# Kernel tuning notes

Measured on AMD Instinct MI355X. Metric: run time of the kernel, lower is better.

Reference implementation:

```python
import jax, jax.numpy as jnp
import numpy as np

D_MODEL = 512; D_STATE = 64; D_CONV = 4; EXPAND = 2; HEADDIM = 64
D_INNER = EXPAND * D_MODEL          # 1024
NHEADS = D_INNER // HEADDIM         # 16
D_IN_PROJ = 2 * D_INNER + 2 * D_STATE + NHEADS  # z, xBC, dt
CONV_DIM = D_INNER + 2 * D_STATE
BETA = 0.5
BATCH = 8; SEQLEN = 1024
EPS_LN = 1e-12; EPS_RMS = 1e-5


def layernorm(x, w, b, eps=EPS_LN):
    mu = jnp.mean(x, axis=-1, keepdims=True)
    var = jnp.var(x, axis=-1, keepdims=True)
    return (x - mu) * jax.lax.rsqrt(var + eps) * w + b


def causal_dw_conv(x, w, b):
    # x: (b, l, c); w: (c, d_conv) depthwise; causal left-pad d_conv-1
    xt = jnp.transpose(x, (0, 2, 1))                 # (b, c, l)
    k = w[:, None, :]                                # (c, 1, d_conv)
    y = jax.lax.conv_general_dilated(
        xt, k, window_strides=(1,), padding=[(D_CONV - 1, 0)],
        feature_group_count=CONV_DIM,
        dimension_numbers=('NCH', 'OIH', 'NCH'))
    return jnp.transpose(y, (0, 2, 1)) + b


def ssd(x, dt, A, Bm, Cm, Dp):
    # x: (b,l,h,p)  dt: (b,l,h)  A: (h)  Bm,Cm: (b,l,n)  Dp: (h)
    dA = jnp.exp(dt * A)  # (b,l,h) decay per step

    def step(h, inp):
        dA_t, dt_t, B_t, C_t, x_t = inp
        # h: (b, heads, p, n)
        h = h * dA_t[:, :, None, None] + jnp.einsum('bh,bn,bhp->bhpn', dt_t, B_t, x_t)
        y = jnp.einsum('bhpn,bn->bhp', h, C_t)
        return h, y

    init = jnp.zeros((x.shape[0], NHEADS, HEADDIM, D_STATE), x.dtype)
    xs = (jnp.moveaxis(dA, 1, 0), jnp.moveaxis(dt, 1, 0),
          jnp.moveaxis(Bm, 1, 0), jnp.moveaxis(Cm, 1, 0), jnp.moveaxis(x, 1, 0))
    _, ys = jax.lax.scan(step, init, xs)
    y = jnp.moveaxis(ys, 0, 1)           # (b,l,h,p)
    return y + x * Dp[None, None, :, None]


def mamba2(u, in_proj_w, conv_w, conv_b, dt_bias, A_log, Dp, norm_w, out_proj_w):
    zxbcdt = u @ in_proj_w.T                                   # (b,l,D_IN_PROJ)
    z, xBC, dt = jnp.split(zxbcdt, [D_INNER, D_INNER + CONV_DIM], axis=-1)
    dt = jax.nn.softplus(dt + dt_bias)                          # (b,l,h)
    xBC = jax.nn.silu(causal_dw_conv(xBC, conv_w, conv_b))
    x, Bm, Cm = jnp.split(xBC, [D_INNER, D_INNER + D_STATE], axis=-1)
    x = x.reshape(x.shape[0], x.shape[1], NHEADS, HEADDIM)
    A = -jnp.exp(A_log)
    y = ssd(x, dt, A, Bm, Cm, Dp)
    y = y.reshape(y.shape[0], y.shape[1], D_INNER)
    g = y * jax.nn.silu(z)                                      # gated RMSNorm
    g = g * jax.lax.rsqrt(jnp.mean(g * g, axis=-1, keepdims=True) + EPS_RMS) * norm_w
    return g @ out_proj_w.T


def ffn(x, w1, b1, w2, b2, lnw, lnb):
    h = jax.nn.gelu(x @ w1.T + b1, approximate=False)
    h = h @ w2.T + b2
    return layernorm(h + x, lnw, lnb)


def setup_inputs() -> dict:
    key = jax.random.key(0)
    ks = jax.random.split(key, 12)
    item_emb = jax.random.normal(ks[0], (BATCH, SEQLEN, D_MODEL), jnp.float32)
    item_idx = jnp.zeros((BATCH, SEQLEN), jnp.int32)          # single sequence per row
    flip_index = jnp.arange(SEQLEN - 1, -1, -1, dtype=jnp.int64)
    s = 0.02
    in_proj_w = jax.random.normal(ks[1], (D_IN_PROJ, D_MODEL), jnp.float32) * s
    conv_w = jax.random.uniform(ks[2], (CONV_DIM, D_CONV), jnp.float32, -0.5, 0.5)
    conv_b = jnp.zeros((CONV_DIM,), jnp.float32)
    # dt_bias = inverse softplus of dt ~ U[1e-3, 0.1] in log space (mamba init)
    dt = jnp.exp(jax.random.uniform(ks[3], (NHEADS,), jnp.float32,
                                    np.log(1e-3), np.log(0.1)))
    dt_bias = dt + jnp.log(-jnp.expm1(-dt))
    A_log = jnp.log(jax.random.uniform(ks[4], (NHEADS,), jnp.float32, 1.0, 16.0))
    Dp = jnp.ones((NHEADS,), jnp.float32)
    norm_w = jnp.ones((D_INNER,), jnp.float32)
    out_proj_w = jax.random.normal(ks[5], (D_MODEL, D_INNER), jnp.float32) * s
    ln_w = jnp.ones((D_MODEL,), jnp.float32); ln_b = jnp.zeros((D_MODEL,), jnp.float32)
    ffn_w1 = jax.random.normal(ks[6], (4 * D_MODEL, D_MODEL), jnp.float32) * s
    ffn_b1 = jnp.zeros((4 * D_MODEL,), jnp.float32)
    ffn_w2 = jax.random.normal(ks[7], (D_MODEL, 4 * D_MODEL), jnp.float32) * s
    ffn_b2 = jnp.zeros((D_MODEL,), jnp.float32)
    ffn_ln_w = jnp.ones((D_MODEL,), jnp.float32); ffn_ln_b = jnp.zeros((D_MODEL,), jnp.float32)
    return dict(item_emb=item_emb, item_idx=item_idx, flip_index=flip_index,
                in_proj_w=in_proj_w, conv_w=conv_w, conv_b=conv_b, dt_bias=dt_bias,
                A_log=A_log, Dp=Dp, norm_w=norm_w, out_proj_w=out_proj_w,
                ln_w=ln_w, ln_b=ln_b, ffn_w1=ffn_w1, ffn_b1=ffn_b1,
                ffn_w2=ffn_w2, ffn_b2=ffn_b2, ffn_ln_w=ffn_ln_w, ffn_ln_b=ffn_ln_b)


def reference(item_emb, item_idx, flip_index, in_proj_w, conv_w, conv_b, dt_bias,
              A_log, Dp, norm_w, out_proj_w, ln_w, ln_b,
              ffn_w1, ffn_b1, ffn_w2, ffn_b2, ffn_ln_w, ffn_ln_b):
    # item_idx (seq_idx) is all-zeros -> no state resets; dropout is eval-mode identity.
    params = (in_proj_w, conv_w, conv_b, dt_bias, A_log, Dp, norm_w, out_proj_w)
    fwd = mamba2(item_emb, *params)
    bwd = mamba2(item_emb[:, flip_index, :], *params)   # shared weights, as in source
    h = fwd + bwd * BETA + item_emb
    h = layernorm(h, ln_w, ln_b)
    return ffn(h, ffn_w1, ffn_b1, ffn_w2, ffn_b2, ffn_ln_w, ffn_ln_b)
```

## Files before the change

### kernel.cpp

```cpp
#include <hip/hip_runtime.h>
#include <math.h>

#define SEQ     1024
#define NBATCH  8
#define NTOK    8192
#define DMODEL  512
#define DINNER  1024
#define NHEADS  16
#define DPROJ   2192
#define DPROJP  2304
#define CONVDIM 1152
#define DFFN    2048

typedef short bf16x8 __attribute__((ext_vector_type(8)));
typedef float f32x4  __attribute__((ext_vector_type(4)));

__device__ inline unsigned short f2bf(float f) {
  union { float f; unsigned int u; } v; v.f = f;
  unsigned int u = v.u;
  return (unsigned short)((u + 0x7FFFu + ((u >> 16) & 1u)) >> 16);
}
__device__ inline float bf2f(unsigned short s) {
  union { unsigned int u; float f; } v; v.u = ((unsigned int)s) << 16;
  return v.f;
}

#define GLDS16(g, l)                                                         \
  __builtin_amdgcn_global_load_lds(                                          \
      (const __attribute__((address_space(1))) unsigned int*)(g),            \
      (__attribute__((address_space(3))) unsigned int*)(l), 16, 0, 0)

__global__ __launch_bounds__(256) void cvt_bf16(const float* __restrict__ s,
                                                unsigned short* __restrict__ d, int n) {
  int i = blockIdx.x * 256 + threadIdx.x;
  if (i < n) d[i] = f2bf(s[i]);
}

__global__ __launch_bounds__(256) void cvt_bf16_pad(const float* __restrict__ s,
                                                    unsigned short* __restrict__ d,
                                                    int realrows, int cols, int padrows) {
  int i = blockIdx.x * 256 + threadIdx.x;
  if (i < padrows * cols) {
    int r = i / cols;
    d[i] = (r < realrows) ? f2bf(s[i]) : (unsigned short)0;
  }
}

template <int MODE>
__global__ __launch_bounds__(256)
void gemm_bt(const unsigned short* __restrict__ A, const unsigned short* __restrict__ B,
             void* __restrict__ Cout, const float* __restrict__ bias,
             float* __restrict__ aux, int Ksub, int lda, int Nreal, size_t zstrideC) {
  __shared__ unsigned short sA[2][128 * 32];
  __shared__ unsigned short sB[2][128 * 32];
  const int tid = threadIdx.x;
  const int bx = blockIdx.x, by = blockIdx.y, bz = blockIdx.z;
  const int lane = tid & 63;
  const int wave = tid >> 6;
  const int wm = wave >> 1, wn = wave & 1;
  const int arow = tid >> 2;
  const int acol = (tid & 3) << 3;

  const unsigned short* pA = A + (size_t)(by * 128 + arow) * lda + bz * Ksub + acol;
  const unsigned short* pB = B + (size_t)(bx * 128 + arow) * lda + bz * Ksub + acol;
  const size_t stride64 = (size_t)64 * lda;
  char* sAw[2] = { (char*)&sA[0][0] + wave * 1024, (char*)&sA[1][0] + wave * 1024 };
  char* sBw[2] = { (char*)&sB[0][0] + wave * 1024, (char*)&sB[1][0] + wave * 1024 };

  f32x4 acc[4][4];
#pragma unroll
  for (int i = 0; i < 4; i++)
#pragma unroll
    for (int j = 0; j < 4; j++) { f32x4 z = {0.f, 0.f, 0.f, 0.f}; acc[i][j] = z; }

  GLDS16(pA, sAw[0]);
  GLDS16(pA + stride64, sAw[0] + 4096);
  GLDS16(pB, sBw[0]);
  GLDS16(pB + stride64, sBw[0] + 4096);
  pA += 32; pB += 32;
  __syncthreads();

  const int lrow = lane & 15;
  const int lkq = (lane >> 4) << 3;
  int cur = 0;
  for (int k0 = 0; k0 < Ksub; k0 += 32) {
    if (k0 + 32 < Ksub) {
      const int nxt = cur ^ 1;
      GLDS16(pA, sAw[nxt]);
      GLDS16(pA + stride64, sAw[nxt] + 4096);
      GLDS16(pB, sBw[nxt]);
      GLDS16(pB + stride64, sBw[nxt] + 4096);
      pA += 32; pB += 32;
    }
    bf16x8 af[4], bfr[4];
#pragma unroll
    for (int mi = 0; mi < 4; mi++)
      af[mi] = *(const bf16x8*)&sA[cur][(wm * 64 + mi * 16 + lrow) * 32 + lkq];
#pragma unroll
    for (int ni = 0; ni < 4; ni++)
      bfr[ni] = *(const bf16x8*)&sB[cur][(wn * 64 + ni * 16 + lrow) * 32 + lkq];
#pragma unroll
    for (int mi = 0; mi < 4; mi++)
#pragma unroll
      for (int ni = 0; ni < 4; ni++)
        acc[mi][ni] = __builtin_amdgcn_mfma_f32_16x16x32_bf16(af[mi], bfr[ni], acc[mi][ni], 0, 0, 0);
    __syncthreads();
    cur ^= 1;
  }

  const int row0 = by * 128 + wm * 64;
  const int col0 = bx * 128 + wn * 64;
  float* outf = (float*)Cout;
  unsigned short* outp16 = (unsigned short*)Cout + (size_t)bz * zstrideC;
#pragma unroll
  for (int mi = 0; mi < 4; mi++) {
#pragma unroll
    for (int ni = 0; ni < 4; ni++) {
      const int col = col0 + ni * 16 + lrow;
      if (col < Nreal) {
        const float bval = (MODE == 0 || MODE == 1) && bias ? bias[col] : 0.f;
#pragma unroll
        for (int r = 0; r < 4; r++) {
          const int row = row0 + mi * 16 + ((lane >> 4) << 2) + r;
          float v = acc[mi][ni][r] + bval;
          if (MODE == 1) {
            float g = 0.5f * v * (1.f + erff(v * 0.7071067811865476f));
            ((unsigned short*)Cout)[(size_t)row * Nreal + col] = f2bf(g);
          } else if (MODE == 2) {
            ((unsigned short*)Cout)[(size_t)row * Nreal + col] = f2bf(v);
            if (col >= 2176) aux[(size_t)row * 16 + (col - 2176)] = v;
          } else if (MODE == 3) {
            outp16[(size_t)row * Nreal + col] = f2bf(v);
          } else {
            outf[(size_t)row * Nreal + col] = v;
          }
        }
      }
    }
  }
}

__global__ __launch_bounds__(256)
void dt_softplus(const float* __restrict__ zdt, const float* __restrict__ dt_bias,
                 float* __restrict__ dtf, float* __restrict__ dtb) {
  int i = blockIdx.x * 256 + threadIdx.x;
  int dir = i >> 17;
  int rem = i & 131071;
  int row = rem >> 10;
  int t = rem & 1023;
  int b = row >> 4, h = row & 15;
  int srow = (b << 10) + (dir ? (1023 - t) : t);
  float v = zdt[(size_t)srow * 16 + h] + dt_bias[h];
  float dt = (v > 20.f) ? v : log1pf(expf(v));
  (dir ? dtb : dtf)[(row << 10) + t] = dt;
}

__global__ __launch_bounds__(256)
void conv_silu_bf(const unsigned short* __restrict__ zxb, const float* __restrict__ cw,
                  const float* __restrict__ cb,
                  unsigned short* __restrict__ xcf, unsigned short* __restrict__ xcb) {
  const int tid = threadIdx.x;
  const int c = blockIdx.x * 128 + (tid & 127);
  const int b = blockIdx.y;
  const int seg = blockIdx.z * 2 + (tid >> 7);
  const int t0 = seg << 5;
  const float w0 = cw[c * 4 + 0], w1 = cw[c * 4 + 1], w2 = cw[c * 4 + 2], w3 = cw[c * 4 + 3];
  const float bias = cb[c];
  const unsigned short* src = zxb + (size_t)(b << 10) * DPROJ + DINNER + c;
  unsigned short* dstf = xcf + (size_t)(b << 10) * CONVDIM + c;
  unsigned short* dstb = xcb + (size_t)(b << 10) * CONVDIM + c;
  float r0 = 0.f, r1 = 0.f, r2 = 0.f;
  if (t0 >= 3) {
    r0 = bf2f(src[(size_t)(t0 - 3) * DPROJ]);
    r1 = bf2f(src[(size_t)(t0 - 2) * DPROJ]);
    r2 = bf2f(src[(size_t)(t0 - 1) * DPROJ]);
  }
  for (int s = t0; s < t0 + 32; s++) {
    float x = bf2f(src[(size_t)s * DPROJ]);
    float vf = bias + w0 * r0 + w1 * r1 + w2 * r2 + w3 * x;
    dstf[(size_t)s * CONVDIM] = f2bf(vf / (1.f + expf(-vf)));
    int tp = 1026 - s;
    if (tp <= 1023) {
      float vb = bias + w0 * x + w1 * r2 + w2 * r1 + w3 * r0;
      dstb[(size_t)tp * CONVDIM] = f2bf(vb / (1.f + expf(-vb)));
    }
    r0 = r1; r1 = r2; r2 = x;
  }
  if (seg == 31) {
    float v2 = bias + w1 * r2 + w2 * r1 + w3 * r0;
    float v1 = bias + w2 * r2 + w3 * r1;
    float v0 = bias + w3 * r2;
    dstb[(size_t)2 * CONVDIM] = f2bf(v2 / (1.f + expf(-v2)));
    dstb[(size_t)1 * CONVDIM] = f2bf(v1 / (1.f + expf(-v1)));
    dstb[0] = f2bf(v0 / (1.f + expf(-v0)));
  }
}

__global__ __launch_bounds__(256)
void ssd_chunk(const unsigned short* __restrict__ xcf, const unsigned short* __restrict__ xcb,
               const float* __restrict__ dtf, const float* __restrict__ dtb,
               const float* __restrict__ A_log, const float* __restrict__ Dp,
               unsigned short* __restrict__ yf, unsigned short* __restrict__ yb) {
  const int blk = blockIdx.x;
  const int dir = blk >> 7;
  const int b = (blk >> 4) & 7;
  const int h = blk & 15;
  const unsigned short* xc = dir ? xcb : xcf;
  const float* dts = (dir ? dtb : dtf) + ((size_t)((b << 4) + h) << 10);
  unsigned short* yo = dir ? yb : yf;
  const float A = -expf(A_log[h]);
  const float Dh = Dp[h];
  const int tid = threadIdx.x;
  const int lane = tid & 63;
  const int w = tid >> 6;
  const int lrow = lane & 15;
  const int quad = lane >> 4;
  const int lk8 = quad << 3;
  const int bS = b << 10;
  const int pr = tid & 31;
  const int sg = tid >> 5;

  __shared__ unsigned short Cb[64 * 72];
  __shared__ unsigned short Bb[64 * 72];
  __shared__ unsigned short Xt[64 * 72];
  __shared__ unsigned short Bt[64 * 72];
  __shared__ unsigned short Mb[64 * 72];
  __shared__ unsigned short Hb[64 * 72];
  __shared__ float sdt_all[1024];

  {
    float4 dv = *(const float4*)(dts + tid * 4);
    *(float4*)&sdt_all[tid * 4] = dv;
  }

  f32x4 hacc[4];
#pragma unroll
  for (int j = 0; j < 4; j++) { f32x4 z = {0.f, 0.f, 0.f, 0.f}; hacc[j] = z; }

  for (int c = 0; c < 16; c++) {
    const int t0 = c << 6;
    __syncthreads();

    float dtl = sdt_all[t0 + lane];
    float v = dtl;
#pragma unroll
    for (int off = 1; off < 64; off <<= 1) {
      float o = __shfl_up(v, off);
      if (lane >= off) v += o;
    }
    const float Lv = A * v;
    const float ev = expf(Lv);
    const float LL = __shfl(Lv, 63);
    const float wv = dtl * expf(LL - Lv);
    const float dtot = expf(LL);

#pragma unroll
    for (int j = 0; j < 4; j++)
#pragma unroll
      for (int r = 0; r < 4; r++)
        Hb[(w * 16 + quad * 4 + r) * 72 + j * 16 + lrow] = f2bf(hacc[j][r]);

#pragma unroll
    for (int pass = 0; pass < 2; pass++) {
      int u = pass * 256 + tid;
      int sl = u >> 3, c8 = u & 7;
      const unsigned short* rowp = xc + (size_t)(bS + t0 + sl) * CONVDIM;
      uint4 vb = *(const uint4*)(rowp + 1024 + c8 * 8);
      uint4 vc = *(const uint4*)(rowp + 1088 + c8 * 8);
      *(uint4*)&Bb[sl * 72 + c8 * 8] = vb;
      *(uint4*)&Cb[sl * 72 + c8 * 8] = vc;
    }

    {
      unsigned int xv[8], bv[8];
      const unsigned short* base = xc + (size_t)(bS + t0 + sg * 8) * CONVDIM;
#pragma unroll
      for (int k = 0; k < 8; k++) {
        const unsigned short* rp = base + (size_t)k * CONVDIM;
        xv[k] = *(const unsigned int*)(rp + h * 64 + pr * 2);
        bv[k] = *(const unsigned int*)(rp + 1024 + pr * 2);
      }
      unsigned short x0[8], x1[8], b0[8], b1[8];
#pragma unroll
      for (int k = 0; k < 8; k++) {
        float ws = __shfl(wv, sg * 8 + k);
        x0[k] = (unsigned short)(xv[k] & 0xffff);
        x1[k] = (unsigned short)(xv[k] >> 16);
        b0[k] = f2bf(bf2f((unsigned short)(bv[k] & 0xffff)) * ws);
        b1[k] = f2bf(bf2f((unsigned short)(bv[k] >> 16)) * ws);
      }
      *(uint4*)&Xt[(pr * 2 + 0) * 72 + sg * 8] = *(const uint4*)x0;
      *(uint4*)&Xt[(pr * 2 + 1) * 72 + sg * 8] = *(const uint4*)x1;
      *(uint4*)&Bt[(pr * 2 + 0) * 72 + sg * 8] = *(const uint4*)b0;
      *(uint4*)&Bt[(pr * 2 + 1) * 72 + sg * 8] = *(const uint4*)b1;
    }
    __syncthreads();

    f32x4 m1[4];
#pragma unroll
    for (int j = 0; j < 4; j++) { f32x4 z = {0.f, 0.f, 0.f, 0.f}; m1[j] = z; }
#pragma unroll
    for (int kq = 0; kq < 2; kq++) {
      bf16x8 af = *(const bf16x8*)&Cb[(w * 16 + lrow) * 72 + kq * 32 + lk8];
#pragma unroll
      for (int j = 0; j < 4; j++) {
        bf16x8 bf = *(const bf16x8*)&Bb[(j * 16 + lrow) * 72 + kq * 32 + lk8];
        m1[j] = __builtin_amdgcn_mfma_f32_16x16x32_bf16(af, bf, m1[j], 0, 0, 0);
      }
    }
#pragma unroll
    for (int r = 0; r < 4; r++) {
      int i = w * 16 + quad * 4 + r;
      float Li = __shfl(Lv, i);
#pragma unroll
      for (int j = 0; j < 4; j++) {
        int s = j * 16 + lrow;
        float Ls = __shfl(Lv, s);
        float ds = __shfl(dtl, s);
        float val = (s <= i) ? m1[j][r] * expf(Li - Ls) * ds : 0.f;
        Mb[i * 72 + s] = f2bf(val);
      }
    }
    __syncthreads();

    f32x4 Y[4], T[4], S[4];
#pragma unroll
    for (int j = 0; j < 4; j++) {
      f32x4 z = {0.f, 0.f, 0.f, 0.f};
      Y[j] = z; T[j] = z; S[j] = z;
    }
#pragma unroll
    for (int kq = 0; kq < 2; kq++) {
      bf16x8 am = *(const bf16x8*)&Mb[(w * 16 + lrow) * 72 + kq * 32 + lk8];
      bf16x8 ac = *(const bf16x8*)&Cb[(w * 16 + lrow) * 72 + kq * 32 + lk8];
      bf16x8 ax = *(const bf16x8*)&Xt[(w * 16 + lrow) * 72 + kq * 32 + lk8];
#pragma unroll
      for (int j = 0; j < 4; j++) {
        bf16x8 bx = *(const bf16x8*)&Xt[(j * 16 + lrow) * 72 + kq * 32 + lk8];
        bf16x8 bh = *(const bf16x8*)&Hb[(j * 16 + lrow) * 72 + kq * 32 + lk8];
        bf16x8 bw = *(const bf16x8*)&Bt[(j * 16 + lrow) * 72 + kq * 32 + lk8];
        Y[j] = __builtin_amdgcn_mfma_f32_16x16x32_bf16(am, bx, Y[j], 0, 0, 0);
        T[j] = __builtin_amdgcn_mfma_f32_16x16x32_bf16(ac, bh, T[j], 0, 0, 0);
        S[j] = __builtin_amdgcn_mfma_f32_16x16x32_bf16(ax, bw, S[j], 0, 0, 0);
      }
    }

#pragma unroll
    for (int r = 0; r < 4; r++) {
      int i = w * 16 + quad * 4 + r;
      float ei = __shfl(ev, i);
#pragma unroll
      for (int j = 0; j < 4; j++) {
        int p = j * 16 + lrow;
        float yv = Y[j][r] + ei * T[j][r] + Dh * bf2f(Xt[p * 72 + i]);
        yo[(size_t)(bS + t0 + i) * DINNER + h * 64 + p] = f2bf(yv);
      }
    }
#pragma unroll
    for (int j = 0; j < 4; j++)
#pragma unroll
      for (int r = 0; r < 4; r++)
        hacc[j][r] = dtot * hacc[j][r] + S[j][r];
  }
}

__device__ inline float2 block_sum2_256(float a, float b) {
#pragma unroll
  for (int o = 32; o >= 1; o >>= 1) { a += __shfl_xor(a, o); b += __shfl_xor(b, o); }
  __shared__ float ra[4], rb[4];
  const int lane = threadIdx.x & 63, w = threadIdx.x >> 6;
  if (lane == 0) { ra[w] = a; rb[w] = b; }
  __syncthreads();
  float2 out;
  out.x = ra[0] + ra[1] + ra[2] + ra[3];
  out.y = rb[0] + rb[1] + rb[2] + rb[3];
  return out;
}

__global__ __launch_bounds__(256)
void gate_rms_comb(const unsigned short* __restrict__ yf, const unsigned short* __restrict__ yb,
                   const unsigned short* __restrict__ zxb, const float* __restrict__ nw,
                   unsigned short* __restrict__ comb) {
  const int bt = blockIdx.x;
  const int b = bt >> 10, t = bt & 1023;
  const int zrowb = (b << 10) + (1023 - t);
  const int tid = threadIdx.x;
  ushort4 yf4 = *(const ushort4*)(yf + (size_t)bt * DINNER + tid * 4);
  ushort4 yb4 = *(const ushort4*)(yb + (size_t)bt * DINNER + tid * 4);
  ushort4 zf4 = *(const ushort4*)(zxb + (size_t)bt * DPROJ + tid * 4);
  ushort4 zb4 = *(const ushort4*)(zxb + (size_t)zrowb * DPROJ + tid * 4);
  float gf[4], gb[4];
  {
    float z0 = bf2f(zf4.x), z1 = bf2f(zf4.y), z2 = bf2f(zf4.z), z3 = bf2f(zf4.w);
    gf[0] = bf2f(yf4.x) * (z0 / (1.f + expf(-z0)));
    gf[1] = bf2f(yf4.y) * (z1 / (1.f + expf(-z1)));
    gf[2] = bf2f(yf4.z) * (z2 / (1.f + expf(-z2)));
    gf[3] = bf2f(yf4.w) * (z3 / (1.f + expf(-z3)));
  }
  {
    float z0 = bf2f(zb4.x), z1 = bf2f(zb4.y), z2 = bf2f(zb4.z), z3 = bf2f(zb4.w);
    gb[0] = bf2f(yb4.x) * (z0 / (1.f + expf(-z0)));
    gb[1] = bf2f(yb4.y) * (z1 / (1.f + expf(-z1)));
    gb[2] = bf2f(yb4.z) * (z2 / (1.f + expf(-z2)));
    gb[3] = bf2f(yb4.w) * (z3 / (1.f + expf(-z3)));
  }
  float2 sr = block_sum2_256(gf[0]*gf[0] + gf[1]*gf[1] + gf[2]*gf[2] + gf[3]*gf[3],
                             gb[0]*gb[0] + gb[1]*gb[1] + gb[2]*gb[2] + gb[3]*gb[3]);
  float sf = rsqrtf(sr.x * (1.f / 1024.f) + 1e-5f);
  float sb = 0.5f * rsqrtf(sr.y * (1.f / 1024.f) + 1e-5f);
  float4 wv = *(const float4*)(nw + tid * 4);
  unsigned short* o = comb + (size_t)bt * DINNER + tid * 4;
  o[0] = f2bf((gf[0] * sf + gb[0] * sb) * wv.x);
  o[1] = f2bf((gf[1] * sf + gb[1] * sb) * wv.y);
  o[2] = f2bf((gf[2] * sf + gb[2] * sb) * wv.z);
  o[3] = f2bf((gf[3] * sf + gb[3] * sb) * wv.w);
}

__global__ __launch_bounds__(256)
void combine_ln(const unsigned short* __restrict__ mo, const float* __restrict__ u,
                const float* __restrict__ w, const float* __restrict__ bias,
                float* __restrict__ hln, unsigned short* __restrict__ hbf) {
  const int bt = blockIdx.x;
  const int tid = threadIdx.x;
  const float2 uu = *(const float2*)(u + (size_t)bt * DMODEL + tid * 2);
  float vx = uu.x, vy = uu.y;
#pragma unroll
  for (int z = 0; z < 4; z++) {
    ushort2 p = *(const ushort2*)(mo + (size_t)z * NTOK * DMODEL + (size_t)bt * DMODEL + tid * 2);
    vx += bf2f(p.x);
    vy += bf2f(p.y);
  }
  float2 sr = block_sum2_256(vx + vy, vx * vx + vy * vy);
  float mean = sr.x * (1.f / 512.f);
  float var = sr.y * (1.f / 512.f) - mean * mean;
  float inv = rsqrtf(var + 1e-12f);
  float2 wv = *(const float2*)(w + tid * 2);
  float2 bv = *(const float2*)(bias + tid * 2);
  float ox = (vx - mean) * inv * wv.x + bv.x;
  float oy = (vy - mean) * inv * wv.y + bv.y;
  *(float2*)(hln + (size_t)bt * DMODEL + tid * 2) = make_float2(ox, oy);
  hbf[(size_t)bt * DMODEL + tid * 2] = f2bf(ox);
  hbf[(size_t)bt * DMODEL + tid * 2 + 1] = f2bf(oy);
}

__global__ __launch_bounds__(256)
void final_ln(const unsigned short* __restrict__ f2, const float* __restrict__ b2,
              const float* __restrict__ hln,
              const float* __restrict__ w, const float* __restrict__ bias,
              float* __restrict__ outp) {
  const int bt = blockIdx.x;
  const int tid = threadIdx.x;
  const float2 bb = *(const float2*)(b2 + tid * 2);
  const float2 h = *(const float2*)(hln + (size_t)bt * DMODEL + tid * 2);
  float vx = bb.x + h.x;
  float vy = bb.y + h.y;
#pragma unroll
  for (int z = 0; z < 4; z++) {
    ushort2 p = *(const ushort2*)(f2 + (size_t)z * NTOK * DMODEL + (size_t)bt * DMODEL + tid * 2);
    vx += bf2f(p.x);
    vy += bf2f(p.y);
  }
  float2 sr = block_sum2_256(vx + vy, vx * vx + vy * vy);
  float mean = sr.x * (1.f / 512.f);
  float var = sr.y * (1.f / 512.f) - mean * mean;
  float inv = rsqrtf(var + 1e-12f);
  float2 wv = *(const float2*)(w + tid * 2);
  float2 bv = *(const float2*)(bias + tid * 2);
  *(float2*)(outp + (size_t)bt * DMODEL + tid * 2) =
      make_float2((vx - mean) * inv * wv.x + bv.x, (vy - mean) * inv * wv.y + bv.y);
}

extern "C" void kernel_launch(void* const* d_in, const int* in_sizes, int n_in,
                              void* d_out, int out_size, void* d_ws, size_t ws_size,
                              hipStream_t stream) {
  const float* item_emb   = (const float*)d_in[0];
  const float* in_proj_w  = (const float*)d_in[3];
  const float* conv_w     = (const float*)d_in[4];
  const float* conv_b     = (const float*)d_in[5];
  const float* dt_bias    = (const float*)d_in[6];
  const float* A_log      = (const float*)d_in[7];
  const float* Dp         = (const float*)d_in[8];
  const float* norm_w     = (const float*)d_in[9];
  const float* out_proj_w = (const float*)d_in[10];
  const float* ln_w       = (const float*)d_in[11];
  const float* ln_b       = (const float*)d_in[12];
  const float* w1         = (const float*)d_in[13];
  const float* b1         = (const float*)d_in[14];
  const float* w2         = (const float*)d_in[15];
  const float* b2         = (const float*)d_in[16];
  const float* fln_w      = (const float*)d_in[17];
  const float* fln_b      = (const float*)d_in[18];
  float* outp = (float*)d_out;
  char* ws = (char*)d_ws;

  const size_t o_ubf  = 0;
  const size_t o_win  = 8388608;
  const size_t o_wout = 10747904;
  const size_t o_w1   = 11796480;
  const size_t o_w2   = 13893632;
  const size_t o_dtf  = 15990784;
  const size_t o_dtb  = 16515072;
  const size_t o_zdt  = 17039360;
  const size_t o_zxb  = 17563648;
  const size_t o_xcf  = 53477376;
  const size_t o_xcb  = 72351744;
  const size_t o_yf   = 91226112;
  const size_t o_yb   = 108003328;
  const size_t o_comb = o_xcf;
  const size_t o_mo   = o_zxb;
  const size_t o_hln  = o_yb;
  const size_t o_hbf  = o_ubf;
  const size_t o_h1   = o_xcb;
  const size_t o_f2   = o_zxb;

  unsigned short* u_bf  = (unsigned short*)(ws + o_ubf);
  unsigned short* winb  = (unsigned short*)(ws + o_win);
  unsigned short* woutb = (unsigned short*)(ws + o_wout);
  unsigned short* w1b   = (unsigned short*)(ws + o_w1);
  unsigned short* w2b   = (unsigned short*)(ws + o_w2);
  float* dtf = (float*)(ws + o_dtf);
  float* dtb = (float*)(ws + o_dtb);
  float* zdt = (float*)(ws + o_zdt);
  unsigned short* zxb = (unsigned short*)(ws + o_zxb);
  unsigned short* xcf = (unsigned short*)(ws + o_xcf);
  unsigned short* xcb = (unsigned short*)(ws + o_xcb);
  unsigned short* yf  = (unsigned short*)(ws + o_yf);
  unsigned short* yb  = (unsigned short*)(ws + o_yb);
  unsigned short* comb = (unsigned short*)(ws + o_comb);
  unsigned short* mo  = (unsigned short*)(ws + o_mo);
  float* hln = (float*)(ws + o_hln);
  unsigned short* hbf = (unsigned short*)(ws + o_hbf);
  unsigned short* h1b = (unsigned short*)(ws + o_h1);
  unsigned short* f2  = (unsigned short*)(ws + o_f2);

  {
    int n = NTOK * DMODEL;
    cvt_bf16<<<(n + 255) / 256, 256, 0, stream>>>(item_emb, u_bf, n);
    cvt_bf16_pad<<<(DPROJP * DMODEL + 255) / 256, 256, 0, stream>>>(in_proj_w, winb, DPROJ, DMODEL, DPROJP);
    n = DMODEL * DINNER;
    cvt_bf16<<<(n + 255) / 256, 256, 0, stream>>>(out_proj_w, woutb, n);
    n = DFFN * DMODEL;
    cvt_bf16<<<(n + 255) / 256, 256, 0, stream>>>(w1, w1b, n);
    n = DMODEL * DFFN;
    cvt_bf16<<<(n + 255) / 256, 256, 0, stream>>>(w2, w2b, n);
  }

  gemm_bt<2><<<dim3(DPROJP / 128, NTOK / 128), 256, 0, stream>>>(
      u_bf, winb, zxb, nullptr, zdt, DMODEL, DMODEL, DPROJ, 0);

  dt_softplus<<<1024, 256, 0, stream>>>(zdt, dt_bias, dtf, dtb);
  conv_silu_bf<<<dim3(9, NBATCH, 16), 256, 0, stream>>>(zxb, conv_w, conv_b, xcf, xcb);

  ssd_chunk<<<256, 256, 0, stream>>>(xcf, xcb, dtf, dtb, A_log, Dp, yf, yb);

  gate_rms_comb<<<NTOK, 256, 0, stream>>>(yf, yb, zxb, norm_w, comb);

  gemm_bt<3><<<dim3(DMODEL / 128, NTOK / 128, 4), 256, 0, stream>>>(
      comb, woutb, mo, nullptr, nullptr, DINNER / 4, DINNER, DMODEL,
      (size_t)NTOK * DMODEL);

  combine_ln<<<NTOK, 256, 0, stream>>>(mo, item_emb, ln_w, ln_b, hln, hbf);

  gemm_bt<1><<<dim3(DFFN / 128, NTOK / 128), 256, 0, stream>>>(
      hbf, w1b, h1b, b1, nullptr, DMODEL, DMODEL, DFFN, 0);

  gemm_bt<3><<<dim3(DMODEL / 128, NTOK / 128, 4), 256, 0, stream>>>(
      h1b, w2b, f2, nullptr, nullptr, DFFN / 4, DFFN, DMODEL,
      (size_t)NTOK * DMODEL);

  final_ln<<<NTOK, 256, 0, stream>>>(f2, b2, hln, fln_w, fln_b, outp);

  (void)in_sizes; (void)n_in; (void)out_size; (void)ws_size;
}
```

Measured before the change: 382.7 us.

## Double-buffer SSD chunk staging and split work across eight waves

The SSD chunk kernel now runs with 512 threads. Each wave computes half the output columns of a 16-row strip. Per-chunk cumsum, decay and weight values for all 16 chunks are computed up front into shared memory, replacing the per-chunk shuffles. The next chunk's B/C/X data is prefetched into registers and written into a second shared-memory buffer while the current chunk computes, which removes one barrier per chunk and hides global load latency. The cost is more shared memory per block and more per-thread register pressure.

Result: faster. 365.6 us (-4.5%).

```diff
diff --git a/kernel.cpp b/kernel.cpp
--- a/kernel.cpp
+++ b/kernel.cpp
@@ -196,7 +196,7 @@
   }
 }
 
-__global__ __launch_bounds__(256)
+__global__ __launch_bounds__(512)
 void ssd_chunk(const unsigned short* __restrict__ xcf, const unsigned short* __restrict__ xcb,
                const float* __restrict__ dtf, const float* __restrict__ dtb,
                const float* __restrict__ A_log, const float* __restrict__ Dp,
@@ -213,35 +213,56 @@
   const int tid = threadIdx.x;
   const int lane = tid & 63;
   const int w = tid >> 6;
+  const int wm = w >> 1;
+  const int wn = w & 1;
   const int lrow = lane & 15;
   const int quad = lane >> 4;
   const int lk8 = quad << 3;
   const int bS = b << 10;
+
+  __shared__ unsigned short Cb[2][64 * 72];
+  __shared__ unsigned short Bb[2][64 * 72];
+  __shared__ unsigned short Xt[2][64 * 72];
+  __shared__ unsigned short Bt[2][64 * 72];
+  __shared__ unsigned short Hb[2][64 * 72];
+  __shared__ unsigned short Mb[64 * 72];
+  __shared__ float sdt_all[1024];
+  __shared__ float Lv_all[16][64];
+  __shared__ float ev_all[16][64];
+  __shared__ float wv_all[16][64];
+  __shared__ float dtot_all[16];
+
+  const unsigned short* bcrow = xc + (size_t)(bS + (tid >> 3)) * CONVDIM + (tid & 7) * 8;
   const int pr = tid & 31;
   const int sg = tid >> 5;
-
-  __shared__ unsigned short Cb[64 * 72];
-  __shared__ unsigned short Bb[64 * 72];
-  __shared__ unsigned short Xt[64 * 72];
-  __shared__ unsigned short Bt[64 * 72];
-  __shared__ unsigned short Mb[64 * 72];
-  __shared__ unsigned short Hb[64 * 72];
-  __shared__ float sdt_all[1024];
-
+  const unsigned short* trow = xc + (size_t)(bS + sg * 4) * CONVDIM;
+
+  uint4 vb, vc;
+  unsigned int xv[4], bv[4];
+
+  vb = *(const uint4*)(bcrow + 1024);
+  vc = *(const uint4*)(bcrow + 1088);
   {
-    float4 dv = *(const float4*)(dts + tid * 4);
-    *(float4*)&sdt_all[tid * 4] = dv;
-  }
-
-  f32x4 hacc[4];
-#pragma unroll
-  for (int j = 0; j < 4; j++) { f32x4 z = {0.f, 0.f, 0.f, 0.f}; hacc[j] = z; }
-
-  for (int c = 0; c < 16; c++) {
-    const int t0 = c << 6;
-    __syncthreads();
-
-    float dtl = sdt_all[t0 + lane];
+    const unsigned short* tp = trow;
+#pragma unroll
+    for (int k = 0; k < 4; k++) {
+      xv[k] = *(const unsigned int*)(tp + h * 64 + pr * 2);
+      bv[k] = *(const unsigned int*)(tp + 1024 + pr * 2);
+      tp += CONVDIM;
+    }
+  }
+
+  *(float2*)&sdt_all[tid * 2] = *(const float2*)(dts + tid * 2);
+  {
+    uint4 z; z.x = 0u; z.y = 0u; z.z = 0u; z.w = 0u;
+    *(uint4*)&Hb[0][(tid >> 3) * 72 + (tid & 7) * 8] = z;
+  }
+  __syncthreads();
+
+#pragma unroll
+  for (int r = 0; r < 2; r++) {
+    const int c = w * 2 + r;
+    float dtl = sdt_all[c * 64 + lane];
     float v = dtl;
 #pragma unroll
     for (int off = 1; off < 64; off <<= 1) {
@@ -249,118 +270,136 @@
       if (lane >= off) v += o;
     }
     const float Lv = A * v;
-    const float ev = expf(Lv);
     const float LL = __shfl(Lv, 63);
-    const float wv = dtl * expf(LL - Lv);
-    const float dtot = expf(LL);
-
-#pragma unroll
-    for (int j = 0; j < 4; j++)
-#pragma unroll
-      for (int r = 0; r < 4; r++)
-        Hb[(w * 16 + quad * 4 + r) * 72 + j * 16 + lrow] = f2bf(hacc[j][r]);
-
-#pragma unroll
-    for (int pass = 0; pass < 2; pass++) {
-      int u = pass * 256 + tid;
-      int sl = u >> 3, c8 = u & 7;
-      const unsigned short* rowp = xc + (size_t)(bS + t0 + sl) * CONVDIM;
-      uint4 vb = *(const uint4*)(rowp + 1024 + c8 * 8);
-      uint4 vc = *(const uint4*)(rowp + 1088 + c8 * 8);
-      *(uint4*)&Bb[sl * 72 + c8 * 8] = vb;
-      *(uint4*)&Cb[sl * 72 + c8 * 8] = vc;
-    }
-
-    {
-      unsigned int xv[8], bv[8];
-      const unsigned short* base = xc + (size_t)(bS + t0 + sg * 8) * CONVDIM;
-#pragma unroll
-      for (int k = 0; k < 8; k++) {
-        const unsigned short* rp = base + (size_t)k * CONVDIM;
-        xv[k] = *(const unsigned int*)(rp + h * 64 + pr * 2);
-        bv[k] = *(const unsigned int*)(rp + 1024 + pr * 2);
-      }
-      unsigned short x0[8], x1[8], b0[8], b1[8];
-#pragma unroll
-      for (int k = 0; k < 8; k++) {
-        float ws = __shfl(wv, sg * 8 + k);
-        x0[k] = (unsigned short)(xv[k] & 0xffff);
-        x1[k] = (unsigned short)(xv[k] >> 16);
-        b0[k] = f2bf(bf2f((unsigned short)(bv[k] & 0xffff)) * ws);
-        b1[k] = f2bf(bf2f((unsigned short)(bv[k] >> 16)) * ws);
-      }
-      *(uint4*)&Xt[(pr * 2 + 0) * 72 + sg * 8] = *(const uint4*)x0;
-      *(uint4*)&Xt[(pr * 2 + 1) * 72 + sg * 8] = *(const uint4*)x1;
-      *(uint4*)&Bt[(pr * 2 + 0) * 72 + sg * 8] = *(const uint4*)b0;
-      *(uint4*)&Bt[(pr * 2 + 1) * 72 + sg * 8] = *(const uint4*)b1;
-    }
-    __syncthreads();
-
-    f32x4 m1[4];
-#pragma unroll
-    for (int j = 0; j < 4; j++) { f32x4 z = {0.f, 0.f, 0.f, 0.f}; m1[j] = z; }
+    Lv_all[c][lane] = Lv;
+    ev_all[c][lane] = expf(Lv);
+    wv_all[c][lane] = dtl * expf(LL - Lv);
+    if (lane == 0) dtot_all[c] = expf(LL);
+  }
+  __syncthreads();
+
+  auto stage_write = [&](int buf, int c) {
+    *(uint4*)&Bb[buf][(tid >> 3) * 72 + (tid & 7) * 8] = vb;
+    *(uint4*)&Cb[buf][(tid >> 3) * 72 + (tid & 7) * 8] = vc;
+    unsigned short x0[4], x1[4], b0[4], b1[4];
+#pragma unroll
+    for (int k = 0; k < 4; k++) {
+      float ws = wv_all[c][sg * 4 + k];
+      x0[k] = (unsigned short)(xv[k] & 0xffff);
+      x1[k] = (unsigned short)(xv[k] >> 16);
+      b0[k] = f2bf(bf2f((unsigned short)(bv[k] & 0xffff)) * ws);
+      b1[k] = f2bf(bf2f((unsigned short)(bv[k] >> 16)) * ws);
+    }
+    *(uint2*)&Xt[buf][(pr * 2 + 0) * 72 + sg * 4] = *(const uint2*)x0;
+    *(uint2*)&Xt[buf][(pr * 2 + 1) * 72 + sg * 4] = *(const uint2*)x1;
+    *(uint2*)&Bt[buf][(pr * 2 + 0) * 72 + sg * 4] = *(const uint2*)b0;
+    *(uint2*)&Bt[buf][(pr * 2 + 1) * 72 + sg * 4] = *(const uint2*)b1;
+  };
+  auto stage_load = [&](int c) {
+    const unsigned short* rp = bcrow + (size_t)c * 64 * CONVDIM;
+    vb = *(const uint4*)(rp + 1024);
+    vc = *(const uint4*)(rp + 1088);
+    const unsigned short* tp = trow + (size_t)c * 64 * CONVDIM;
+#pragma unroll
+    for (int k = 0; k < 4; k++) {
+      xv[k] = *(const unsigned int*)(tp + h * 64 + pr * 2);
+      bv[k] = *(const unsigned int*)(tp + 1024 + pr * 2);
+      tp += CONVDIM;
+    }
+  };
+
+  stage_write(0, 0);
+  stage_load(1);
+  __syncthreads();
+
+  f32x4 hacc[2];
+#pragma unroll
+  for (int j = 0; j < 2; j++) { f32x4 z = {0.f, 0.f, 0.f, 0.f}; hacc[j] = z; }
+
+  int cur = 0;
+  for (int c = 0; c < 16; c++) {
+    const int t0 = c << 6;
+
+    f32x4 m1[2];
+#pragma unroll
+    for (int j = 0; j < 2; j++) { f32x4 z = {0.f, 0.f, 0.f, 0.f}; m1[j] = z; }
 #pragma unroll
     for (int kq = 0; kq < 2; kq++) {
-      bf16x8 af = *(const bf16x8*)&Cb[(w * 16 + lrow) * 72 + kq * 32 + lk8];
-#pragma unroll
-      for (int j = 0; j < 4; j++) {
-        bf16x8 bf = *(const bf16x8*)&Bb[(j * 16 + lrow) * 72 + kq * 32 + lk8];
+      bf16x8 af = *(const bf16x8*)&Cb[cur][(wm * 16 + lrow) * 72 + kq * 32 + lk8];
+#pragma unroll
+      for (int j = 0; j < 2; j++) {
+        bf16x8 bf = *(const bf16x8*)&Bb[cur][(wn * 32 + j * 16 + lrow) * 72 + kq * 32 + lk8];
         m1[j] = __builtin_amdgcn_mfma_f32_16x16x32_bf16(af, bf, m1[j], 0, 0, 0);
       }
     }
 #pragma unroll
     for (int r = 0; r < 4; r++) {
-      int i = w * 16 + quad * 4 + r;
-      float Li = __shfl(Lv, i);
-#pragma unroll
-      for (int j = 0; j < 4; j++) {
-        int s = j * 16 + lrow;
-        float Ls = __shfl(Lv, s);
-        float ds = __shfl(dtl, s);
+      const int i = wm * 16 + quad * 4 + r;
+      const float Li = Lv_all[c][i];
+#pragma unroll
+      for (int j = 0; j < 2; j++) {
+        const int s = wn * 32 + j * 16 + lrow;
+        const float Ls = Lv_all[c][s];
+        const float ds = sdt_all[c * 64 + s];
         float val = (s <= i) ? m1[j][r] * expf(Li - Ls) * ds : 0.f;
         Mb[i * 72 + s] = f2bf(val);
       }
     }
     __syncthreads();
 
-    f32x4 Y[4], T[4], S[4];
-#pragma unroll
-    for (int j = 0; j < 4; j++) {
+    f32x4 Y[2], T[2], S[2];
+#pragma unroll
+    for (int j = 0; j < 2; j++) {
       f32x4 z = {0.f, 0.f, 0.f, 0.f};
       Y[j] = z; T[j] = z; S[j] = z;
     }
 #pragma unroll
     for (int kq = 0; kq < 2; kq++) {
-      bf16x8 am = *(const bf16x8*)&Mb[(w * 16 + lrow) * 72 + kq * 32 + lk8];
-      bf16x8 ac = *(const bf16x8*)&Cb[(w * 16 + lrow) * 72 + kq * 32 + lk8];
-      bf16x8 ax = *(const bf16x8*)&Xt[(w * 16 + lrow) * 72 + kq * 32 + lk8];
-#pragma unroll
-      for (int j = 0; j < 4; j++) {
-        bf16x8 bx = *(const bf16x8*)&Xt[(j * 16 + lrow) * 72 + kq * 32 + lk8];
-        bf16x8 bh = *(const bf16x8*)&Hb[(j * 16 + lrow) * 72 + kq * 32 + lk8];
-        bf16x8 bw = *(const bf16x8*)&Bt[(j * 16 + lrow) * 72 + kq * 32 + lk8];
+      bf16x8 am = *(const bf16x8*)&Mb[(wm * 16 + lrow) * 72 + kq * 32 + lk8];
+      bf16x8 ac = *(const bf16x8*)&Cb[cur][(wm * 16 + lrow) * 72 + kq * 32 + lk8];
+      bf16x8 ax = *(const bf16x8*)&Xt[cur][(wm * 16 + lrow) * 72 + kq * 32 + lk8];
+#pragma unroll
+      for (int j = 0; j < 2; j++) {
+        const int brow = (wn * 32 + j * 16 + lrow) * 72 + kq * 32 + lk8;
+        bf16x8 bx = *(const bf16x8*)&Xt[cur][brow];
+        bf16x8 bh = *(const bf16x8*)&Hb[cur][brow];
+        bf16x8 bw = *(const bf16x8*)&Bt[cur][brow];
         Y[j] = __builtin_amdgcn_mfma_f32_16x16x32_bf16(am, bx, Y[j], 0, 0, 0);
         T[j] = __builtin_amdgcn_mfma_f32_16x16x32_bf16(ac, bh, T[j], 0, 0, 0);
         S[j] = __builtin_amdgcn_mfma_f32_16x16x32_bf16(ax, bw, S[j], 0, 0, 0);
       }
     }
 
+    const float dtot = dtot_all[c];
 #pragma unroll
     for (int r = 0; r < 4; r++) {
-      int i = w * 16 + quad * 4 + r;
-      float ei = __shfl(ev, i);
-#pragma unroll
-      for (int j = 0; j < 4; j++) {
-        int p = j * 16 + lrow;
-        float yv = Y[j][r] + ei * T[j][r] + Dh * bf2f(Xt[p * 72 + i]);
+      const int i = wm * 16 + quad * 4 + r;
+      const float ei = ev_all[c][i];
+#pragma unroll
+      for (int j = 0; j < 2; j++) {
+        const int p = wn * 32 + j * 16 + lrow;
+        float yv = Y[j][r] + ei * T[j][r] + Dh * bf2f(Xt[cur][p * 72 + i]);
         yo[(size_t)(bS + t0 + i) * DINNER + h * 64 + p] = f2bf(yv);
       }
     }
 #pragma unroll
-    for (int j = 0; j < 4; j++)
+    for (int j = 0; j < 2; j++)
 #pragma unroll
       for (int r = 0; r < 4; r++)
         hacc[j][r] = dtot * hacc[j][r] + S[j][r];
+
+    const int nxt = cur ^ 1;
+    if (c + 1 < 16) {
+#pragma unroll
+      for (int j = 0; j < 2; j++)
+#pragma unroll
+        for (int r = 0; r < 4; r++)
+          Hb[nxt][(wm * 16 + quad * 4 + r) * 72 + wn * 32 + j * 16 + lrow] = f2bf(hacc[j][r]);
+      stage_write(nxt, c + 1);
+      if (c + 2 < 16) stage_load(c + 2);
+    }
+    __syncthreads();
+    cur = nxt;
   }
 }
 
@@ -551,7 +590,7 @@
   dt_softplus<<<1024, 256, 0, stream>>>(zdt, dt_bias, dtf, dtb);
   conv_silu_bf<<<dim3(9, NBATCH, 16), 256, 0, stream>>>(zxb, conv_w, conv_b, xcf, xcb);
 
-  ssd_chunk<<<256, 256, 0, stream>>>(xcf, xcb, dtf, dtb, A_log, Dp, yf, yb);
+  ssd_chunk<<<256, 512, 0, stream>>>(xcf, xcb, dtf, dtb, A_log, Dp, yf, yb);
 
   gate_rms_comb<<<NTOK, 256, 0, stream>>>(yf, yb, zxb, norm_w, comb);
 
```
